# Performance work log

Measured on AMD Instinct MI355X. Metric: run time of the kernel, lower is better.

## Reference

```python
import jax, jax.numpy as jnp
import numpy as np
from jax import lax

B, IN_CH, OUT_CH, H, W = 32, 128, 256, 64, 64
STYLE_CH, TDIM, G = 512, 512, 32
GN_EPS, MOD_EPS = 1e-5, 1e-8
DN = ('NCHW', 'OIHW', 'NCHW')


def swish(x):
    return x * jax.nn.sigmoid(x)


def group_norm(x, gamma, beta):
    n, c, h, w = x.shape
    xr = x.reshape(n, G, c // G, h, w)
    mu = xr.mean(axis=(2, 3, 4), keepdims=True)
    var = xr.var(axis=(2, 3, 4), keepdims=True)
    xn = ((xr - mu) * lax.rsqrt(var + GN_EPS)).reshape(n, c, h, w)
    return xn * gamma[None, :, None, None] + beta[None, :, None, None]


def conv3x3(x, w, b):
    y = lax.conv_general_dilated(x, w, (1, 1), ((1, 1), (1, 1)), dimension_numbers=DN)
    return y + b[None, :, None, None]


def setup_inputs() -> dict:
    key = jax.random.key(0)
    ks = jax.random.split(key, 16)
    s = 0.05
    return {
        'x': jax.random.normal(ks[0], (B, IN_CH, H, W), jnp.float32),
        'temb': jax.random.normal(ks[1], (B, TDIM), jnp.float32),
        'style': jax.random.normal(ks[2], (B, STYLE_CH), jnp.float32),
        'gn1_g': jnp.ones((IN_CH,), jnp.float32),
        'gn1_b': jnp.zeros((IN_CH,), jnp.float32),
        'conv1_w': jax.random.normal(ks[3], (OUT_CH, IN_CH, 3, 3), jnp.float32) * s,
        'conv1_b': jnp.zeros((OUT_CH,), jnp.float32),
        'temb_w': jax.random.normal(ks[4], (OUT_CH, TDIM), jnp.float32) * s,
        'temb_b': jnp.zeros((OUT_CH,), jnp.float32),
        'gn2_g': jnp.ones((OUT_CH,), jnp.float32),
        'gn2_b': jnp.zeros((OUT_CH,), jnp.float32),
        'style_w': jax.random.normal(ks[5], (OUT_CH, STYLE_CH), jnp.float32) * s,
        'style_b': jnp.zeros((OUT_CH,), jnp.float32),
        'mod_w': jax.random.normal(ks[6], (OUT_CH, OUT_CH, 3, 3), jnp.float32) * s,
        'sc_w': jax.random.normal(ks[7], (OUT_CH, IN_CH, 1, 1), jnp.float32) * s,
        'sc_b': jnp.zeros((OUT_CH,), jnp.float32),
    }


def reference(x, temb, style, gn1_g, gn1_b, conv1_w, conv1_b, temb_w, temb_b,
              gn2_g, gn2_b, style_w, style_b, mod_w, sc_w, sc_b):
    # block1: GN -> Swish -> Conv3x3
    h = conv3x3(swish(group_norm(x, gn1_g, gn1_b)), conv1_w, conv1_b)
    # temb projection: Swish -> Linear, broadcast over HxW
    h = h + (swish(temb) @ temb_w.T + temb_b)[:, :, None, None]
    # block2: GN -> Swish -> Dropout(0) [identity]
    h = swish(group_norm(h, gn2_g, gn2_b))
    # modulated + demodulated per-sample conv (StyleGAN2-style)
    style2 = style @ style_w.T + style_b                       # (b, out_ch)
    wmod = mod_w[None] * (style2[:, None, :, None, None] + 1.0)  # (b, o, i, kh, kw)
    d = lax.rsqrt((wmod ** 2).sum(axis=(2, 3, 4), keepdims=True) + MOD_EPS)
    wmod = wmod * d
    conv1s = lambda xi, wi: lax.conv_general_dilated(
        xi[None], wi, (1, 1), ((1, 1), (1, 1)), dimension_numbers=DN)[0]
    h = jax.vmap(conv1s)(h, wmod)                              # per-sample conv
    # shortcut 1x1 conv (in_ch != out_ch)
    sc = lax.conv_general_dilated(x, sc_w, (1, 1), ((0, 0), (0, 0)), dimension_numbers=DN)
    sc = sc + sc_b[None, :, None, None]
    return h + sc
```

## Files before the change

### kernel.cpp

```cpp
#include <hip/hip_runtime.h>
#include <cstdint>

typedef unsigned short u16;
typedef unsigned int   u32;

typedef __attribute__((ext_vector_type(8))) short bf16x8;
typedef __attribute__((ext_vector_type(4))) float f32x4;

#define DEV __device__ __forceinline__

static constexpr int HP = 66, WP = 66;

DEV u16 f2bf(float f) {
  u32 u = __float_as_uint(f);
  u32 r = (u + 0x7fffu + ((u >> 16) & 1u)) >> 16;
  return (u16)r;
}
DEV float bf2f(u16 v) { return __uint_as_float((u32)v << 16); }

DEV void gload_lds16(const void* g, void* s) {
  __builtin_amdgcn_global_load_lds(
      (const __attribute__((address_space(1))) void*)g,
      (__attribute__((address_space(3))) void*)s, 16, 0, 0);
}

__global__ __launch_bounds__(256) void repack_w_kernel(const float* __restrict__ src,
                                                       u16* __restrict__ dst,
                                                       int Cin, int K, int total,
                                                       int ksq, int kdim) {
  for (int idx = blockIdx.x * 256 + threadIdx.x; idx < total; idx += gridDim.x * 256) {
    int co = idx / K;
    int r  = idx - co * K;
    int s  = r / Cin;
    int ci = r - s * Cin;
    int ky = s / kdim, kx = s - ky * kdim;
    dst[idx] = f2bf(src[(co * Cin + ci) * ksq + ky * kdim + kx]);
  }
}

__global__ __launch_bounds__(256) void modw_ss_kernel(const float* __restrict__ w,
                                                      float* __restrict__ SS_T) {
  int o = blockIdx.x, i = threadIdx.x;
  const float* p = w + (size_t)(o * 256 + i) * 9;
  float s = 0.f;
#pragma unroll
  for (int k = 0; k < 9; ++k) s += p[k] * p[k];
  SS_T[i * 256 + o] = s;
}

__global__ __launch_bounds__(256) void style_mvec_kernel(const float* __restrict__ style,
                                                         const float* __restrict__ style_w,
                                                         const float* __restrict__ style_b,
                                                         float* __restrict__ mvec) {
  __shared__ float st[512];
  int b = blockIdx.x, t = threadIdx.x;
  for (int k = t; k < 512; k += 256) st[k] = style[b * 512 + k];
  __syncthreads();
  const float4* wr = (const float4*)(style_w + t * 512);
  float acc = 0.f;
  for (int k = 0; k < 128; ++k) {
    float4 w4 = wr[k];
    acc += w4.x * st[k*4] + w4.y * st[k*4+1] + w4.z * st[k*4+2] + w4.w * st[k*4+3];
  }
  mvec[b * 256 + t] = acc + style_b[t] + 1.f;
}

__global__ __launch_bounds__(256) void demod_kernel(const float* __restrict__ mvec,
                                                    const float* __restrict__ SS_T,
                                                    float* __restrict__ dvec) {
  __shared__ float m2[256];
  int b = blockIdx.x, t = threadIdx.x;
  float mv = mvec[b * 256 + t];
  m2[t] = mv * mv;
  __syncthreads();
  float acc = 0.f;
  for (int i = 0; i < 256; ++i) acc += m2[i] * SS_T[i * 256 + t];
  dvec[b * 256 + t] = rsqrtf(acc + 1e-8f);
}

__global__ __launch_bounds__(256) void scale_sc_kernel(const float* __restrict__ sc_w,
                                                       const float* __restrict__ dvec,
                                                       u16* __restrict__ scTb) {
  int idx = blockIdx.x * 256 + threadIdx.x;
  int ci = idx & 127;
  int co = (idx >> 7) & 255;
  int b  = idx >> 15;
  scTb[idx] = f2bf(sc_w[co * 128 + ci] / dvec[b * 256 + co]);
}

__global__ __launch_bounds__(256) void temb_proj_kernel(const float* __restrict__ temb,
                                                        const float* __restrict__ temb_w,
                                                        const float* __restrict__ temb_b,
                                                        const float* __restrict__ conv1_b,
                                                        float* __restrict__ tb2) {
  __shared__ float sw[512];
  int b = blockIdx.x, t = threadIdx.x;
  for (int k = t; k < 512; k += 256) {
    float v = temb[b * 512 + k];
    sw[k] = v / (1.f + __expf(-v));
  }
  __syncthreads();
  const float4* wr = (const float4*)(temb_w + t * 512);
  float acc = 0.f;
  for (int k = 0; k < 128; ++k) {
    float4 w4 = wr[k];
    acc += w4.x * sw[k*4] + w4.y * sw[k*4+1] + w4.z * sw[k*4+2] + w4.w * sw[k*4+3];
  }
  tb2[b * 256 + t] = acc + temb_b[t] + conv1_b[t];
}

template <int C>
__global__ __launch_bounds__(256) void halo_zero_kernel(u16* __restrict__ buf) {
  int idx = blockIdx.x * 256 + threadIdx.x;
  const int GR = C / 8;
  if (idx >= 32 * 260 * GR) return;
  int g = idx % GR;
  int p = (idx / GR) % 260;
  int b = idx / (GR * 260);
  int y, x;
  if (p < 66)       { y = 0;        x = p; }
  else if (p < 132) { y = 65;       x = p - 66; }
  else if (p < 196) { y = p - 131;  x = 0; }
  else              { y = p - 195;  x = 65; }
  uint4 z; z.x = 0; z.y = 0; z.z = 0; z.w = 0;
  *(uint4*)(buf + (((size_t)b * HP + y) * WP + x) * C + g * 8) = z;
}

__global__ __launch_bounds__(256) void gn1_stats_kernel(const float* __restrict__ x,
                                                        float2* __restrict__ st1) {
  int bg = blockIdx.x;
  const float4* p = (const float4*)(x + (size_t)bg * 16384);
  float s = 0.f, s2 = 0.f;
  for (int i = threadIdx.x; i < 4096; i += 256) {
    float4 v = p[i];
    s  += v.x + v.y + v.z + v.w;
    s2 += v.x*v.x + v.y*v.y + v.z*v.z + v.w*v.w;
  }
  for (int d = 32; d; d >>= 1) { s += __shfl_down(s, d); s2 += __shfl_down(s2, d); }
  __shared__ float red[2][4];
  if ((threadIdx.x & 63) == 0) { red[0][threadIdx.x >> 6] = s; red[1][threadIdx.x >> 6] = s2; }
  __syncthreads();
  if (threadIdx.x == 0) {
    s  = red[0][0] + red[0][1] + red[0][2] + red[0][3];
    s2 = red[1][0] + red[1][1] + red[1][2] + red[1][3];
    float mean = s / 16384.f;
    float var  = s2 / 16384.f - mean * mean;
    st1[bg] = make_float2(mean, rsqrtf(var + 1e-5f));
  }
}

__global__ __launch_bounds__(256) void gn1_apply_kernel(const float* __restrict__ x,
                                                        const float2* __restrict__ st1,
                                                        const float* __restrict__ g1,
                                                        const float* __restrict__ b1,
                                                        u16* __restrict__ act1p,
                                                        u16* __restrict__ xh) {
  __shared__ float xs[128][65];
  int blk = blockIdx.x;
  int b = blk >> 6, y = blk & 63;
  int t = threadIdx.x;
#pragma unroll 8
  for (int pass = 0; pass < 32; ++pass) {
    int c = pass * 4 + (t >> 6);
    xs[c][t & 63] = x[(((size_t)b * 128 + c) * 64 + y) * 64 + (t & 63)];
  }
  __syncthreads();
  for (int pass = 0; pass < 32; ++pass) {
    int xc = pass * 2 + (t >> 7);
    int c  = t & 127;
    float v = xs[c][xc];
    float2 ms = st1[b * 32 + (c >> 2)];
    float vn = (v - ms.x) * ms.y * g1[c] + b1[c];
    float sw = vn / (1.f + __expf(-vn));
    act1p[(((size_t)b * HP + (y + 1)) * WP + (xc + 1)) * 128 + c] = f2bf(sw);
    xh[(((size_t)b * 64 + y) * 64 + xc) * 128 + c] = f2bf(v);
  }
}

__global__ __launch_bounds__(256) void gn2_part_kernel(const u16* __restrict__ h1,
                                                       float2* __restrict__ part) {
  int b = blockIdx.x >> 4, chunk = blockIdx.x & 15;
  int t = threadIdx.x;
  int g = t & 31, sub = t >> 5;
  float s = 0.f, s2 = 0.f;
  const u16* base = h1 + ((size_t)b * 4096 + chunk * 256) * 256 + g * 8;
  for (int pp = 0; pp < 32; ++pp) {
    uint4 raw = *(const uint4*)(base + (size_t)(pp * 8 + sub) * 256);
    const u16* rs = (const u16*)&raw;
#pragma unroll
    for (int e = 0; e < 8; ++e) { float v = bf2f(rs[e]); s += v; s2 += v * v; }
  }
  s += __shfl_xor(s, 32); s2 += __shfl_xor(s2, 32);
  __shared__ float red[2][4][32];
  int wv = t >> 6, ln = t & 63;
  if (ln < 32) { red[0][wv][ln] = s; red[1][wv][ln] = s2; }
  __syncthreads();
  if (t < 32) {
    float ts  = red[0][0][t] + red[0][1][t] + red[0][2][t] + red[0][3][t];
    float ts2 = red[1][0][t] + red[1][1][t] + red[1][2][t] + red[1][3][t];
    part[(b * 16 + chunk) * 32 + t] = make_float2(ts, ts2);
  }
}

__global__ void gn2_final_kernel(const float2* __restrict__ part, float2* __restrict__ st2) {
  int idx = blockIdx.x * 256 + threadIdx.x;
  if (idx >= 1024) return;
  int b = idx >> 5, g = idx & 31;
  float s = 0.f, s2 = 0.f;
  for (int c = 0; c < 16; ++c) { float2 p = part[(b * 16 + c) * 32 + g]; s += p.x; s2 += p.y; }
  float mean = s / 32768.f;
  float var  = s2 / 32768.f - mean * mean;
  st2[idx] = make_float2(mean, rsqrtf(var + 1e-5f));
}

__global__ __launch_bounds__(256) void gn2_apply_kernel(const u16* __restrict__ h1,
                                                        const float2* __restrict__ st2,
                                                        const float* __restrict__ g2,
                                                        const float* __restrict__ b2,
                                                        const float* __restrict__ mvec,
                                                        u16* __restrict__ act2p) {
  int idx = blockIdx.x * 256 + threadIdx.x;
  int gpix = idx >> 5;
  int gi = idx & 31;
  int c0 = gi * 8;
  int b = gpix >> 12, y = (gpix >> 6) & 63, x = gpix & 63;
  uint4 raw = *(const uint4*)(h1 + (size_t)gpix * 256 + c0);
  const u16* rs = (const u16*)&raw;
  float2 ms = st2[b * 32 + gi];
  const float* mv = mvec + b * 256 + c0;
  u16 outp[8];
#pragma unroll
  for (int e = 0; e < 8; ++e) {
    float v  = bf2f(rs[e]);
    float vn = (v - ms.x) * ms.y * g2[c0 + e] + b2[c0 + e];
    float sw = vn / (1.f + __expf(-vn));
    outp[e] = f2bf(sw * mv[e]);
  }
  *(uint4*)(act2p + (((size_t)b * HP + (y + 1)) * WP + (x + 1)) * 256 + c0) = *(const uint4*)outp;
}

template <int MODE>
__global__ __launch_bounds__(512, 2) void igemm_kernel(const u16* __restrict__ act,
                                                       const u16* __restrict__ wT,
                                                       const float* __restrict__ epi,
                                                       const u16* __restrict__ xh,
                                                       const u16* __restrict__ scTb,
                                                       const float* __restrict__ sc_b,
                                                       u16* __restrict__ h1out,
                                                       float* __restrict__ fout) {
  constexpr int CIN    = (MODE == 0) ? 128 : 256;
  constexpr int NSUB   = CIN / 64;
  constexpr int KW     = CIN * 9;
  constexpr int NKMAIN = KW / 64;
  constexpr int NKT    = (MODE == 2) ? NKMAIN + 2 : NKMAIN;

  __shared__ __align__(16) unsigned char lds[131072];
  const int tid  = threadIdx.x;
  const int wave = tid >> 6, lane = tid & 63;
  const int wm = wave >> 2, wn = wave & 3;
  const int m_base = blockIdx.x * 256;
  const int bimg = m_base >> 12;
  const int ln = lane & 15, l4 = lane >> 4;

  const int srow = lane >> 3;
  const int glog = (lane & 7) ^ srow;

  u32 pixA[2][2], pixX[2][2], rowB[2][2], rowS[2][2];
#pragma unroll
  for (int j = 0; j < 2; ++j)
#pragma unroll
    for (int h = 0; h < 2; ++h) {
      int mlocal = (wave & 3) * 16 + j * 8 + srow + h * 64 + (wave >> 2) * 128;
      int m = m_base + mlocal;
      int y = (m >> 6) & 63, x = m & 63;
      pixA[j][h] = (u32)((bimg * HP + y) * WP + x) * CIN + glog * 8;
      if (MODE == 2) pixX[j][h] = (u32)m * 128 + glog * 8;
      int co = (wave >> 1) * 64 + h * 32 + (wave & 1) * 16 + j * 8 + srow;
      rowB[j][h] = (u32)co * KW + glog * 8;
      if (MODE == 2) rowS[j][h] = (u32)(bimg * 256 + co) * 128 + glog * 8;
    }

  f32x4 acc[8][4];
#pragma unroll
  for (int i = 0; i < 8; ++i)
#pragma unroll
    for (int j = 0; j < 4; ++j) acc[i][j] = (f32x4){0.f, 0.f, 0.f, 0.f};

  auto stageA = [&](int kt, int h, int buf) {
    unsigned char* dst = lds + buf * 65536 + h * 16384 + wave * 2048;
    if (MODE == 2 && kt >= NKMAIN) {
      u32 ko = (u32)(kt - NKMAIN) * 64;
      gload_lds16(xh + pixX[0][h] + ko, dst);
      gload_lds16(xh + pixX[1][h] + ko, dst + 1024);
    } else {
      int tap = kt / NSUB;
      int kin = (kt - tap * NSUB) * 64;
      int ky = tap / 3, kx = tap - ky * 3;
      u32 ko = (u32)((ky * WP + kx) * CIN + kin);
      gload_lds16(act + pixA[0][h] + ko, dst);
      gload_lds16(act + pixA[1][h] + ko, dst + 1024);
    }
  };
  auto stageB = [&](int kt, int g, int buf) {
    unsigned char* dst = lds + buf * 65536 + 32768 + g * 16384 + wave * 2048;
    if (MODE == 2 && kt >= NKMAIN) {
      u32 ko = (u32)(kt - NKMAIN) * 64;
      gload_lds16(scTb + rowS[0][g] + ko, dst);
      gload_lds16(scTb + rowS[1][g] + ko, dst + 1024);
    } else {
      u32 ko = (u32)kt * 64;
      gload_lds16(wT + rowB[0][g] + ko, dst);
      gload_lds16(wT + rowB[1][g] + ko, dst + 1024);
    }
  };

  bf16x8 af[8], bf[4];
  auto ldA = [&](int h, int buf) {
    const unsigned char* As = lds + buf * 65536;
#pragma unroll
    for (int f = 0; f < 4; ++f)
#pragma unroll
      for (int kk = 0; kk < 2; ++kk) {
        int lr = h * 128 + wm * 64 + f * 16 + ln;
        int gr = (kk * 4 + l4) ^ (ln & 7);
        af[f * 2 + kk] = *(const bf16x8*)(As + lr * 128 + gr * 16);
      }
  };
  auto ldB = [&](int g, int buf) {
    const unsigned char* Bs = lds + buf * 65536 + 32768;
#pragma unroll
    for (int f1 = 0; f1 < 2; ++f1)
#pragma unroll
      for (int kk = 0; kk < 2; ++kk) {
        int lr = g * 128 + wn * 32 + f1 * 16 + ln;
        int gr = (kk * 4 + l4) ^ (ln & 7);
        bf[f1 * 2 + kk] = *(const bf16x8*)(Bs + lr * 128 + gr * 16);
      }
  };
  auto mmac = [&](int h, int g) {
    __builtin_amdgcn_s_setprio(1);
#pragma unroll
    for (int f = 0; f < 4; ++f)
#pragma unroll
      for (int f1 = 0; f1 < 2; ++f1)
#pragma unroll
        for (int kk = 0; kk < 2; ++kk)
          acc[h * 4 + f][g * 2 + f1] = __builtin_amdgcn_mfma_f32_16x16x32_bf16(
              af[f * 2 + kk], bf[f1 * 2 + kk], acc[h * 4 + f][g * 2 + f1], 0, 0, 0);
    __builtin_amdgcn_s_setprio(0);
  };

#define PHASE_BAR() do { __builtin_amdgcn_sched_barrier(0); \
    __builtin_amdgcn_s_barrier(); __builtin_amdgcn_sched_barrier(0); } while (0)

  stageA(0, 0, 0); stageB(0, 0, 0); stageB(0, 1, 0); stageA(0, 1, 0);

#pragma unroll 2
  for (int kt = 0; kt < NKT - 1; ++kt) {
    const int cur = kt & 1, nxt = cur ^ 1;
    stageA(kt + 1, 0, nxt);
    asm volatile("s_waitcnt vmcnt(6)" ::: "memory");
    PHASE_BAR();
    ldB(0, cur); ldA(0, cur);
    mmac(0, 0);
    stageB(kt + 1, 0, nxt);
    asm volatile("s_waitcnt vmcnt(6)" ::: "memory");
    PHASE_BAR();
    ldB(1, cur);
    mmac(0, 1);
    stageB(kt + 1, 1, nxt);
    asm volatile("s_waitcnt vmcnt(6)" ::: "memory");
    PHASE_BAR();
    ldA(1, cur);
    mmac(1, 1);
    stageA(kt + 1, 1, nxt);
    PHASE_BAR();
    ldB(0, cur);
    mmac(1, 0);
  }
  {
    const int cur = (NKT - 1) & 1;
    asm volatile("s_waitcnt vmcnt(4)" ::: "memory");
    PHASE_BAR();
    ldB(0, cur); ldA(0, cur); mmac(0, 0);
    asm volatile("s_waitcnt vmcnt(2)" ::: "memory");
    PHASE_BAR();
    ldB(1, cur); mmac(0, 1);
    asm volatile("s_waitcnt vmcnt(0)" ::: "memory");
    PHASE_BAR();
    ldA(1, cur); mmac(1, 1);
    PHASE_BAR();
    ldB(0, cur); mmac(1, 0);
  }
#undef PHASE_BAR

  if (MODE == 0) {
    const float* tbrow = epi + bimg * 256;
#pragma unroll
    for (int fm = 0; fm < 8; ++fm)
#pragma unroll
      for (int fn = 0; fn < 4; ++fn) {
        int co = wn * 64 + fn * 16 + ln;
        float add = tbrow[co];
#pragma unroll
        for (int i = 0; i < 4; ++i) {
          int m = m_base + wm * 128 + fm * 16 + (l4 << 2) + i;
          h1out[(size_t)m * 256 + co] = f2bf(acc[fm][fn][i] + add);
        }
      }
  } else {
    float* tile = (float*)lds;
    const int pixb = m_base & 4095;
#pragma unroll
    for (int c = 0; c < 4; ++c) {
      __syncthreads();
      if (wn == c) {
#pragma unroll
        for (int fn = 0; fn < 4; ++fn) {
          int nl = fn * 16 + ln;
          int co = c * 64 + nl;
          float dsc = epi[bimg * 256 + co];
          float scb = sc_b[co];
#pragma unroll
          for (int fm = 0; fm < 8; ++fm)
#pragma unroll
            for (int i = 0; i < 4; ++i) {
              int ml = wm * 128 + fm * 16 + (l4 << 2) + i;
              tile[nl * 257 + ml] = acc[fm][fn][i] * dsc + scb;
            }
        }
      }
      __syncthreads();
#pragma unroll 4
      for (int it = 0; it < 32; ++it) {
        int lin = it * 512 + tid;
        int co_l = lin >> 8, ml = lin & 255;
        fout[((size_t)(bimg * 256 + c * 64 + co_l)) * 4096 + pixb + ml] =
            tile[co_l * 257 + ml];
      }
    }
  }
}

extern "C" void kernel_launch(void* const* d_in, const int* in_sizes, int n_in,
                              void* d_out, int out_size, void* d_ws, size_t ws_size,
                              hipStream_t stream) {
  const float* x       = (const float*)d_in[0];
  const float* temb    = (const float*)d_in[1];
  const float* style   = (const float*)d_in[2];
  const float* gn1_g   = (const float*)d_in[3];
  const float* gn1_b   = (const float*)d_in[4];
  const float* conv1_w = (const float*)d_in[5];
  const float* conv1_b = (const float*)d_in[6];
  const float* temb_w  = (const float*)d_in[7];
  const float* temb_b  = (const float*)d_in[8];
  const float* gn2_g   = (const float*)d_in[9];
  const float* gn2_b   = (const float*)d_in[10];
  const float* style_w = (const float*)d_in[11];
  const float* style_b = (const float*)d_in[12];
  const float* mod_w   = (const float*)d_in[13];
  const float* sc_w    = (const float*)d_in[14];
  const float* sc_b    = (const float*)d_in[15];
  float* out = (float*)d_out;
  char* ws = (char*)d_ws;

  size_t o = 0;
  auto alloc = [&](size_t bytes) { size_t r = o; o += (bytes + 255) & ~(size_t)255; return r; };
  const size_t act1p_bytes = (size_t)32 * HP * WP * 128 * 2;
  const size_t xh_bytes    = (size_t)32 * 64 * 64 * 128 * 2;
  const size_t h1_bytes    = (size_t)32 * 4096 * 256 * 2;
  const size_t act2p_bytes = (size_t)32 * HP * WP * 256 * 2;
  size_t o_act1p = alloc(act1p_bytes);
  size_t o_xh    = alloc(xh_bytes);
  size_t o_h1    = alloc(h1_bytes);
  size_t o_act2p = alloc(act2p_bytes);
  size_t o_w1T   = alloc((size_t)256 * 1152 * 2);
  size_t o_wmT   = alloc((size_t)256 * 2304 * 2);
  size_t o_scTb  = alloc((size_t)32 * 256 * 128 * 2);
  size_t o_tb2   = alloc(8192 * 4);
  size_t o_mvec  = alloc(8192 * 4);
  size_t o_dvec  = alloc(8192 * 4);
  size_t o_SS    = alloc((size_t)256 * 256 * 4);
  size_t o_st1   = alloc(1024 * 8);
  size_t o_st2   = alloc(1024 * 8);
  size_t o_part  = alloc(512 * 32 * 8);
  if (ws_size < o) return;

  u16*    act1p = (u16*)(ws + o_act1p);
  u16*    xh    = (u16*)(ws + o_xh);
  u16*    h1    = (u16*)(ws + o_h1);
  u16*    act2p = (u16*)(ws + o_act2p);
  u16*    w1T   = (u16*)(ws + o_w1T);
  u16*    wmT   = (u16*)(ws + o_wmT);
  u16*    scTb  = (u16*)(ws + o_scTb);
  float*  tb2   = (float*)(ws + o_tb2);
  float*  mvec  = (float*)(ws + o_mvec);
  float*  dvec  = (float*)(ws + o_dvec);
  float*  SS_T  = (float*)(ws + o_SS);
  float2* st1   = (float2*)(ws + o_st1);
  float2* st2   = (float2*)(ws + o_st2);
  float2* part  = (float2*)(ws + o_part);

  halo_zero_kernel<128><<<(32 * 260 * 16 + 255) / 256, 256, 0, stream>>>(act1p);
  halo_zero_kernel<256><<<(32 * 260 * 32 + 255) / 256, 256, 0, stream>>>(act2p);

  repack_w_kernel<<<1152, 256, 0, stream>>>(conv1_w, w1T, 128, 1152, 256 * 1152, 9, 3);
  repack_w_kernel<<<2304, 256, 0, stream>>>(mod_w, wmT, 256, 2304, 256 * 2304, 9, 3);
  modw_ss_kernel<<<256, 256, 0, stream>>>(mod_w, SS_T);
  temb_proj_kernel<<<32, 256, 0, stream>>>(temb, temb_w, temb_b, conv1_b, tb2);
  style_mvec_kernel<<<32, 256, 0, stream>>>(style, style_w, style_b, mvec);
  demod_kernel<<<32, 256, 0, stream>>>(mvec, SS_T, dvec);
  scale_sc_kernel<<<4096, 256, 0, stream>>>(sc_w, dvec, scTb);
  gn1_stats_kernel<<<1024, 256, 0, stream>>>(x, st1);
  gn1_apply_kernel<<<2048, 256, 0, stream>>>(x, st1, gn1_g, gn1_b, act1p, xh);

  igemm_kernel<0><<<512, 512, 0, stream>>>(act1p, w1T, tb2, nullptr, nullptr,
                                           nullptr, h1, nullptr);

  gn2_part_kernel<<<512, 256, 0, stream>>>(h1, part);
  gn2_final_kernel<<<4, 256, 0, stream>>>(part, st2);
  gn2_apply_kernel<<<16384, 256, 0, stream>>>(h1, st2, gn2_g, gn2_b, mvec, act2p);

  igemm_kernel<2><<<512, 512, 0, stream>>>(act2p, wmT, dvec, xh, scTb,
                                           sc_b, nullptr, out);
}
```

Baseline: 373.5 us.

## Fuse GN2 statistics into conv1 epilogue, restructure GEMM pipeline, swizzle block order

Conv1's epilogue now accumulates per-group sum and sum of squares of its fp32 outputs and adds them atomically into a small buffer. This removes the separate GN2 partial-reduction kernel and its full reread of h1. The main GEMM loop is reordered to issue LDS reads before the barrier with explicit lgkmcnt waits, and the peeled final iteration is folded into the loop behind a `more` flag. Block indices are swizzled so adjacent launches touch different images. The stats now come from pre-rounding fp32 values and are summed with nondeterministic float atomics, and the buffer must be zeroed with a memset each call.

```diff
diff --git a/kernel.cpp b/kernel.cpp
--- a/kernel.cpp
+++ b/kernel.cpp
@@ -177,37 +177,11 @@
   }
 }
 
-__global__ __launch_bounds__(256) void gn2_part_kernel(const u16* __restrict__ h1,
-                                                       float2* __restrict__ part) {
-  int b = blockIdx.x >> 4, chunk = blockIdx.x & 15;
-  int t = threadIdx.x;
-  int g = t & 31, sub = t >> 5;
-  float s = 0.f, s2 = 0.f;
-  const u16* base = h1 + ((size_t)b * 4096 + chunk * 256) * 256 + g * 8;
-  for (int pp = 0; pp < 32; ++pp) {
-    uint4 raw = *(const uint4*)(base + (size_t)(pp * 8 + sub) * 256);
-    const u16* rs = (const u16*)&raw;
-#pragma unroll
-    for (int e = 0; e < 8; ++e) { float v = bf2f(rs[e]); s += v; s2 += v * v; }
-  }
-  s += __shfl_xor(s, 32); s2 += __shfl_xor(s2, 32);
-  __shared__ float red[2][4][32];
-  int wv = t >> 6, ln = t & 63;
-  if (ln < 32) { red[0][wv][ln] = s; red[1][wv][ln] = s2; }
-  __syncthreads();
-  if (t < 32) {
-    float ts  = red[0][0][t] + red[0][1][t] + red[0][2][t] + red[0][3][t];
-    float ts2 = red[1][0][t] + red[1][1][t] + red[1][2][t] + red[1][3][t];
-    part[(b * 16 + chunk) * 32 + t] = make_float2(ts, ts2);
-  }
-}
-
-__global__ void gn2_final_kernel(const float2* __restrict__ part, float2* __restrict__ st2) {
+__global__ void gn2_final_kernel(const float* __restrict__ st2sum, float2* __restrict__ st2) {
   int idx = blockIdx.x * 256 + threadIdx.x;
   if (idx >= 1024) return;
-  int b = idx >> 5, g = idx & 31;
-  float s = 0.f, s2 = 0.f;
-  for (int c = 0; c < 16; ++c) { float2 p = part[(b * 16 + c) * 32 + g]; s += p.x; s2 += p.y; }
+  float s  = st2sum[idx * 2];
+  float s2 = st2sum[idx * 2 + 1];
   float mean = s / 32768.f;
   float var  = s2 / 32768.f - mean * mean;
   st2[idx] = make_float2(mean, rsqrtf(var + 1e-5f));
@@ -247,7 +221,8 @@
                                                        const u16* __restrict__ scTb,
                                                        const float* __restrict__ sc_b,
                                                        u16* __restrict__ h1out,
-                                                       float* __restrict__ fout) {
+                                                       float* __restrict__ fout,
+                                                       float* __restrict__ st2sum) {
   constexpr int CIN    = (MODE == 0) ? 128 : 256;
   constexpr int NSUB   = CIN / 64;
   constexpr int KW     = CIN * 9;
@@ -258,7 +233,8 @@
   const int tid  = threadIdx.x;
   const int wave = tid >> 6, lane = tid & 63;
   const int wm = wave >> 2, wn = wave & 3;
-  const int m_base = blockIdx.x * 256;
+  const int swz = ((blockIdx.x & 7) << 6) | (blockIdx.x >> 3);
+  const int m_base = swz * 256;
   const int bimg = m_base >> 12;
   const int ln = lane & 15, l4 = lane >> 4;
 
@@ -350,52 +326,51 @@
     __builtin_amdgcn_s_setprio(0);
   };
 
-#define PHASE_BAR() do { __builtin_amdgcn_sched_barrier(0); \
-    __builtin_amdgcn_s_barrier(); __builtin_amdgcn_sched_barrier(0); } while (0)
+#define SB() __builtin_amdgcn_sched_barrier(0)
+#define LGKM0() asm volatile("s_waitcnt lgkmcnt(0)" ::: "memory")
 
   stageA(0, 0, 0); stageB(0, 0, 0); stageB(0, 1, 0); stageA(0, 1, 0);
+  asm volatile("s_waitcnt vmcnt(4)" ::: "memory");
+  __builtin_amdgcn_s_barrier();
 
 #pragma unroll 2
-  for (int kt = 0; kt < NKT - 1; ++kt) {
+  for (int kt = 0; kt < NKT; ++kt) {
     const int cur = kt & 1, nxt = cur ^ 1;
-    stageA(kt + 1, 0, nxt);
-    asm volatile("s_waitcnt vmcnt(6)" ::: "memory");
-    PHASE_BAR();
-    ldB(0, cur); ldA(0, cur);
+    const bool more = (kt + 1 < NKT);
+    ldB(0, cur); ldA(0, cur); SB();
+    if (more) { stageA(kt + 1, 0, nxt);
+                asm volatile("s_waitcnt vmcnt(4)" ::: "memory"); }
+    else      { asm volatile("s_waitcnt vmcnt(2)" ::: "memory"); }
+    __builtin_amdgcn_s_barrier();
+    LGKM0(); SB();
     mmac(0, 0);
-    stageB(kt + 1, 0, nxt);
-    asm volatile("s_waitcnt vmcnt(6)" ::: "memory");
-    PHASE_BAR();
-    ldB(1, cur);
+    ldB(1, cur); SB();
+    if (more) { stageB(kt + 1, 0, nxt);
+                asm volatile("s_waitcnt vmcnt(4)" ::: "memory"); }
+    else      { asm volatile("s_waitcnt vmcnt(0)" ::: "memory"); }
+    __builtin_amdgcn_s_barrier();
+    LGKM0(); SB();
     mmac(0, 1);
-    stageB(kt + 1, 1, nxt);
-    asm volatile("s_waitcnt vmcnt(6)" ::: "memory");
-    PHASE_BAR();
-    ldA(1, cur);
+    ldA(1, cur); SB();
+    if (more) stageB(kt + 1, 1, nxt);
+    __builtin_amdgcn_s_barrier();
+    LGKM0(); SB();
     mmac(1, 1);
-    stageA(kt + 1, 1, nxt);
-    PHASE_BAR();
-    ldB(0, cur);
+    ldB(0, cur); SB();
+    if (more) { stageA(kt + 1, 1, nxt);
+                asm volatile("s_waitcnt vmcnt(4)" ::: "memory"); }
+    __builtin_amdgcn_s_barrier();
+    LGKM0(); SB();
     mmac(1, 0);
   }
-  {
-    const int cur = (NKT - 1) & 1;
-    asm volatile("s_waitcnt vmcnt(4)" ::: "memory");
-    PHASE_BAR();
-    ldB(0, cur); ldA(0, cur); mmac(0, 0);
-    asm volatile("s_waitcnt vmcnt(2)" ::: "memory");
-    PHASE_BAR();
-    ldB(1, cur); mmac(0, 1);
-    asm volatile("s_waitcnt vmcnt(0)" ::: "memory");
-    PHASE_BAR();
-    ldA(1, cur); mmac(1, 1);
-    PHASE_BAR();
-    ldB(0, cur); mmac(1, 0);
-  }
-#undef PHASE_BAR
+#undef SB
+#undef LGKM0
 
   if (MODE == 0) {
     const float* tbrow = epi + bimg * 256;
+    float ps[4], ps2[4];
+#pragma unroll
+    for (int fn = 0; fn < 4; ++fn) { ps[fn] = 0.f; ps2[fn] = 0.f; }
 #pragma unroll
     for (int fm = 0; fm < 8; ++fm)
 #pragma unroll
@@ -405,9 +380,25 @@
 #pragma unroll
         for (int i = 0; i < 4; ++i) {
           int m = m_base + wm * 128 + fm * 16 + (l4 << 2) + i;
-          h1out[(size_t)m * 256 + co] = f2bf(acc[fm][fn][i] + add);
+          float v = acc[fm][fn][i] + add;
+          h1out[(size_t)m * 256 + co] = f2bf(v);
+          ps[fn] += v; ps2[fn] += v * v;
         }
       }
+#pragma unroll
+    for (int fn = 0; fn < 4; ++fn) {
+      float s = ps[fn], s2 = ps2[fn];
+      s += __shfl_xor(s, 1);  s2 += __shfl_xor(s2, 1);
+      s += __shfl_xor(s, 2);  s2 += __shfl_xor(s2, 2);
+      s += __shfl_xor(s, 4);  s2 += __shfl_xor(s2, 4);
+      s += __shfl_xor(s, 16); s2 += __shfl_xor(s2, 16);
+      s += __shfl_xor(s, 32); s2 += __shfl_xor(s2, 32);
+      if ((lane & 55) == 0) {
+        int g = wn * 8 + fn * 2 + (ln >> 3);
+        atomicAdd(&st2sum[bimg * 64 + g * 2 + 0], s);
+        atomicAdd(&st2sum[bimg * 64 + g * 2 + 1], s2);
+      }
+    }
   } else {
     float* tile = (float*)lds;
     const int pixb = m_base & 4095;
@@ -483,7 +474,7 @@
   size_t o_SS    = alloc((size_t)256 * 256 * 4);
   size_t o_st1   = alloc(1024 * 8);
   size_t o_st2   = alloc(1024 * 8);
-  size_t o_part  = alloc(512 * 32 * 8);
+  size_t o_s2sum = alloc(32 * 32 * 2 * 4);
   if (ws_size < o) return;
 
   u16*    act1p = (u16*)(ws + o_act1p);
@@ -499,10 +490,11 @@
   float*  SS_T  = (float*)(ws + o_SS);
   float2* st1   = (float2*)(ws + o_st1);
   float2* st2   = (float2*)(ws + o_st2);
-  float2* part  = (float2*)(ws + o_part);
+  float*  s2sum = (float*)(ws + o_s2sum);
 
   halo_zero_kernel<128><<<(32 * 260 * 16 + 255) / 256, 256, 0, stream>>>(act1p);
   halo_zero_kernel<256><<<(32 * 260 * 32 + 255) / 256, 256, 0, stream>>>(act2p);
+  hipMemsetAsync(s2sum, 0, 32 * 32 * 2 * 4, stream);
 
   repack_w_kernel<<<1152, 256, 0, stream>>>(conv1_w, w1T, 128, 1152, 256 * 1152, 9, 3);
   repack_w_kernel<<<2304, 256, 0, stream>>>(mod_w, wmT, 256, 2304, 256 * 2304, 9, 3);
@@ -515,12 +507,11 @@
   gn1_apply_kernel<<<2048, 256, 0, stream>>>(x, st1, gn1_g, gn1_b, act1p, xh);
 
   igemm_kernel<0><<<512, 512, 0, stream>>>(act1p, w1T, tb2, nullptr, nullptr,
-                                           nullptr, h1, nullptr);
-
-  gn2_part_kernel<<<512, 256, 0, stream>>>(h1, part);
-  gn2_final_kernel<<<4, 256, 0, stream>>>(part, st2);
+                                           nullptr, h1, nullptr, s2sum);
+
+  gn2_final_kernel<<<4, 256, 0, stream>>>(s2sum, st2);
   gn2_apply_kernel<<<16384, 256, 0, stream>>>(h1, st2, gn2_g, gn2_b, mvec, act2p);
 
   igemm_kernel<2><<<512, 512, 0, stream>>>(act2p, wmT, dvec, xh, scTb,
-                                           sc_b, nullptr, out);
-}
+                                           sc_b, nullptr, out, nullptr);
+}
```

After: 538.1 us. 44.1% more time.
